# Kernel tuning notes

Measured on AMD Instinct MI355X. Metric: run time of the kernel, lower is better.

The kernel has to match this reference:

```python
import jax, jax.numpy as jnp
import numpy as np

L = 4        # routed layers
E = 12       # experts
NH = 4       # attention heads
C = 256      # hidden_dim
M = 128      # mlp_dim
TOPK = 1
LN_EPS = 1e-5


def setup_inputs() -> dict:
    key = jax.random.key(0)
    ks = jax.random.split(key, 16)
    B, H, W = 128, 14, 14

    def w(k, shape, s=0.02):
        return jax.random.normal(k, shape, dtype=jnp.float32) * s

    return {
        'stem_out': jax.random.normal(ks[0], (B, C, H, W), dtype=jnp.float32),
        'gate_w': w(ks[1], (L, C, E)), 'gate_b': jnp.zeros((L, E), jnp.float32),
        'ln1_g': jnp.ones((L, E, C), jnp.float32), 'ln1_b': jnp.zeros((L, E, C), jnp.float32),
        'wq': w(ks[2], (L, E, C, C)), 'bq': jnp.zeros((L, E, C), jnp.float32),
        'wk': w(ks[3], (L, E, C, C)), 'bk': jnp.zeros((L, E, C), jnp.float32),
        'wv': w(ks[4], (L, E, C, C)), 'bv': jnp.zeros((L, E, C), jnp.float32),
        'wo': w(ks[5], (L, E, C, C)), 'bo': jnp.zeros((L, E, C), jnp.float32),
        'ln2_g': jnp.ones((L, E, C), jnp.float32), 'ln2_b': jnp.zeros((L, E, C), jnp.float32),
        'w1': w(ks[6], (L, E, C, M)), 'b1': jnp.zeros((L, E, M), jnp.float32),
        'w2': w(ks[7], (L, E, M, C)), 'b2': jnp.zeros((L, E, C), jnp.float32),
    }


def _ln(x, g, b):
    mu = x.mean(axis=-1, keepdims=True)
    var = ((x - mu) ** 2).mean(axis=-1, keepdims=True)
    return (x - mu) * jax.lax.rsqrt(var + LN_EPS) * g + b


def _vit_block(x, p):
    # x: (B, H, W, C); p: per-expert params (no expert axis)
    B, H, W, Cc = x.shape
    d = Cc // NH
    h = _ln(x, p['g1'], p['bb1'])
    q = h @ p['wq'] + p['bq']
    k = h @ p['wk'] + p['bk']
    v = h @ p['wv'] + p['bv']

    def split(t):  # (B,H,W,C) -> (B, NH, H, W, d)
        return jnp.transpose(t.reshape(B, H, W, NH, d), (0, 3, 1, 2, 4))

    q, k, v = split(q), split(k), split(v)
    # attention is computed PER ROW h (over the W axis), matching the
    # original matmul(q, k.transpose(-2,-1)) on b n h w d tensors
    scale = jnp.asarray(d, x.dtype) ** 0.5
    scores = jnp.einsum('bnhqd,bnhkd->bnhqk', q, k) / scale
    attn = jax.nn.softmax(scores, axis=-1)
    o = jnp.einsum('bnhqk,bnhkd->bnhqd', attn, v)
    o = jnp.transpose(o, (0, 2, 3, 1, 4)).reshape(B, H, W, Cc)
    o = o @ p['wo'] + p['bo']
    x = x + o
    m = _ln(x, p['g2'], p['bb2'])
    m = jax.nn.gelu(m @ p['w1'] + p['b1'], approximate=False) @ p['w2'] + p['b2']
    return x + m


def reference(stem_out, gate_w, gate_b, ln1_g, ln1_b, wq, bq, wk, bk, wv, bv,
              wo, bo, ln2_g, ln2_b, w1, b1, w2, b2):
    x = jnp.transpose(stem_out, (0, 2, 3, 1))  # (B, H, W, C)
    B = x.shape[0]
    outputs_map, probs_list, idx_list = [], [], []
    for li in range(L):
        router_in = x.mean(axis=(1, 2))                 # (B, C)
        logits = router_in @ gate_w[li] + gate_b[li]    # (B, E)
        all_probs = jax.nn.softmax(logits, axis=-1)
        tk_p, tk_i = jax.lax.top_k(all_probs, TOPK)
        tk_p = tk_p / (tk_p.sum(axis=-1, keepdims=True) + 1e-8)
        # dense combine weights (B, E): scatter top-k weights per batch row
        w_be = jnp.zeros((B, E), x.dtype).at[jnp.arange(B)[:, None], tk_i].add(tk_p)
        p_li = {'g1': ln1_g[li], 'bb1': ln1_b[li],
                'wq': wq[li], 'bq': bq[li], 'wk': wk[li], 'bk': bk[li],
                'wv': wv[li], 'bv': bv[li], 'wo': wo[li], 'bo': bo[li],
                'g2': ln2_g[li], 'bb2': ln2_b[li],
                'w1': w1[li], 'b1': b1[li], 'w2': w2[li], 'b2': b2[li]}
        expert_outs = jax.vmap(lambda pp: _vit_block(x, pp))(p_li)  # (E,B,H,W,C)
        x = jnp.einsum('ebhwc,be->bhwc', expert_outs, w_be)
        outputs_map.append(jax.lax.stop_gradient(x))
        probs_list.append(all_probs)
        idx_list.append(tk_i)
    return (jnp.stack(outputs_map, axis=0),          # (4, B, H, W, C)
            jnp.concatenate(probs_list, axis=0),     # (4B, E)
            jnp.concatenate(idx_list, axis=0))       # (4B, top_k)
```

## Files before the change

### kernel.cpp

```cpp
#include <hip/hip_runtime.h>
#include <hip/hip_bf16.h>

#define LNUM 4
#define ENUM 12
#define CH 256
#define MLP 128
#define HW 196
#define BNUM 128
#define ROWLEN 14
#define MTOT (BNUM * HW)
#define MAXT128 208
#define MAXT64 416

#define PK_WQ 0
#define PK_WK 786432
#define PK_WV 1572864
#define PK_WO 2359296
#define PK_W1 3145728
#define PK_W2 3538944
#define PK_TOTAL 3932160

using bf16x8 = __attribute__((ext_vector_type(8))) short;
using f32x4 = __attribute__((ext_vector_type(4))) float;

__device__ inline unsigned short f2bf(float v) {
  __hip_bfloat16 b = __float2bfloat16(v);
  return *reinterpret_cast<unsigned short*>(&b);
}
__device__ inline float bf2f(unsigned short u) {
  union { unsigned int i; float f; } cv;
  cv.i = ((unsigned int)u) << 16;
  return cv.f;
}
__device__ inline void split_bf(float v, unsigned short& hi, unsigned short& lo) {
  hi = f2bf(v);
  lo = f2bf(v - bf2f(hi));
}
__device__ inline void gload16(const void* g, void* l) {
  __builtin_amdgcn_global_load_lds(
      (const __attribute__((address_space(1))) unsigned int*)g,
      (__attribute__((address_space(3))) unsigned int*)l, 16, 0, 0);
}

__global__ __launch_bounds__(256) void transpose_stem(const float* __restrict__ stem,
                                                      float* __restrict__ x,
                                                      int* __restrict__ rcnt) {
  if (blockIdx.x == 0 && blockIdx.y == 0 && blockIdx.z == 0 &&
      threadIdx.x == 0 && threadIdx.y == 0)
    rcnt[0] = 0;
  __shared__ float tile[32][33];
  int b = blockIdx.z;
  int c0 = blockIdx.x * 32;
  int p0 = blockIdx.y * 32;
  int tx = threadIdx.x;
  int ty = threadIdx.y;
  for (int i = ty; i < 32; i += 8) {
    int c = c0 + i, p = p0 + tx;
    if (p < HW) tile[i][tx] = stem[(size_t)b * CH * HW + (size_t)c * HW + p];
  }
  __syncthreads();
  for (int i = ty; i < 32; i += 8) {
    int p = p0 + i, c = c0 + tx;
    if (p < HW) x[(size_t)b * HW * CH + (size_t)p * CH + c] = tile[tx][i];
  }
}

__global__ __launch_bounds__(256) void router_kernel(
    const float* __restrict__ x, const float* __restrict__ gate_w,
    const float* __restrict__ gate_b, float* __restrict__ probs_out,
    float* __restrict__ idx_out, float* __restrict__ weight,
    int* __restrict__ eidx, int* __restrict__ rcnt, int* __restrict__ perm,
    int* __restrict__ te128, int* __restrict__ tr0128, int* __restrict__ trw128,
    int* __restrict__ te64, int* __restrict__ tr064, int* __restrict__ trw64,
    int li) {
  int b = blockIdx.x;
  int tid = threadIdx.x;
  int w = tid >> 6, lane = tid & 63;
  const float* xb = x + (size_t)b * HW * CH;
  float a0 = 0.f, a1 = 0.f, a2 = 0.f, a3 = 0.f;
#pragma unroll 7
  for (int i = 0; i < 49; ++i) {
    int p = w * 49 + i;
    float4 vv = *reinterpret_cast<const float4*>(&xb[(size_t)p * CH + lane * 4]);
    a0 += vv.x; a1 += vv.y; a2 += vv.z; a3 += vv.w;
  }
  __shared__ float rsum[4][CH];
  rsum[w][lane * 4 + 0] = a0;
  rsum[w][lane * 4 + 1] = a1;
  rsum[w][lane * 4 + 2] = a2;
  rsum[w][lane * 4 + 3] = a3;
  __syncthreads();
  __shared__ float r[CH];
  r[tid] = (rsum[0][tid] + rsum[1][tid] + rsum[2][tid] + rsum[3][tid]) *
           (1.0f / (float)HW);
  __syncthreads();
  __shared__ float part[ENUM][16];
  if (tid < 192) {
    int e = tid >> 4, seg = tid & 15;
    const float* gw = gate_w + (size_t)li * CH * ENUM;
    float acc = 0.f;
#pragma unroll
    for (int kk = 0; kk < 16; ++kk) {
      int k = seg * 16 + kk;
      acc += r[k] * gw[(size_t)k * ENUM + e];
    }
    part[e][seg] = acc;
  }
  __syncthreads();
  __shared__ float logits[ENUM];
  if (tid < ENUM) {
    float acc = gate_b[li * ENUM + tid];
#pragma unroll
    for (int seg = 0; seg < 16; ++seg) acc += part[tid][seg];
    logits[tid] = acc;
  }
  __syncthreads();
  __shared__ int last;
  if (tid == 0) {
    float mx = logits[0]; int am = 0;
    for (int e = 1; e < ENUM; ++e) if (logits[e] > mx) { mx = logits[e]; am = e; }
    float pr[ENUM]; float den = 0.f;
    for (int e = 0; e < ENUM; ++e) { pr[e] = expf(logits[e] - mx); den += pr[e]; }
    float inv = 1.0f / den;
    for (int e = 0; e < ENUM; ++e) pr[e] *= inv;
    for (int e = 0; e < ENUM; ++e)
      probs_out[(size_t)(li * BNUM + b) * ENUM + e] = pr[e];
    idx_out[li * BNUM + b] = (float)am;
    float pmax = pr[am];
    weight[b] = pmax / (pmax + 1e-8f);
    eidx[b] = am;
    __threadfence();
    int old = atomicAdd(rcnt, 1);
    last = (old == BNUM - 1) ? 1 : 0;
  }
  __syncthreads();
  if (!last) return;
  __threadfence();
  __shared__ int cnt[ENUM], start[ENUM];
  int t = tid;
  if (t < ENUM) {
    int cc = 0;
    for (int bb = 0; bb < BNUM; ++bb) if (eidx[bb] == t) ++cc;
    cnt[t] = cc;
  }
  __syncthreads();
  if (t == 0) {
    int ss = 0;
    for (int e = 0; e < ENUM; ++e) { start[e] = ss; ss += cnt[e]; }
  }
  __syncthreads();
  if (t < ENUM) {
    int pos = start[t];
    for (int bb = 0; bb < BNUM; ++bb) if (eidx[bb] == t) perm[pos++] = bb;
  }
  if (t == 0) {
    int tile = 0;
    for (int e = 0; e < ENUM; ++e) {
      int rows = cnt[e] * HW;
      int row0 = start[e] * HW;
      int off = 0;
      while (off < rows) {
        te128[tile] = e;
        tr0128[tile] = row0 + off;
        int rem = rows - off;
        trw128[tile] = rem < 128 ? rem : 128;
        ++tile; off += 128;
      }
    }
    for (; tile < MAXT128; ++tile) { trw128[tile] = 0; te128[tile] = 0; tr0128[tile] = 0; }
    rcnt[0] = 0;
  } else if (t == 1) {
    int tile = 0;
    for (int e = 0; e < ENUM; ++e) {
      int rows = cnt[e] * HW;
      int row0 = start[e] * HW;
      int off = 0;
      while (off < rows) {
        te64[tile] = e;
        tr064[tile] = row0 + off;
        int rem = rows - off;
        trw64[tile] = rem < 64 ? rem : 64;
        ++tile; off += 64;
      }
    }
    for (; tile < MAXT64; ++tile) { trw64[tile] = 0; te64[tile] = 0; tr064[tile] = 0; }
  }
}

__global__ __launch_bounds__(256) void prepack(
    const float* __restrict__ wq, const float* __restrict__ wk,
    const float* __restrict__ wv, const float* __restrict__ wo,
    const float* __restrict__ w1, const float* __restrict__ w2,
    unsigned short* __restrict__ Phi, unsigned short* __restrict__ Plo,
    int li0, int plane_mult) {
  int lz = blockIdx.z / ENUM;
  int e = blockIdx.z % ENUM;
  int li = li0 + lz;
  size_t plane = (size_t)lz * plane_mult;
  int ts = blockIdx.y;
  int K = (ts == 5) ? 128 : 256;
  int N = (ts == 4) ? 128 : 256;
  int total = (K / 8) * N;
  int id = blockIdx.x * 256 + threadIdx.x;
  if (id >= total) return;
  const float* src;
  size_t dst0;
  switch (ts) {
    case 0: src = wq; dst0 = PK_WQ; break;
    case 1: src = wk; dst0 = PK_WK; break;
    case 2: src = wv; dst0 = PK_WV; break;
    case 3: src = wo; dst0 = PK_WO; break;
    case 4: src = w1; dst0 = PK_W1; break;
    default: src = w2; dst0 = PK_W2; break;
  }
  src += ((size_t)li * ENUM + e) * K * N;
  size_t dst = plane + dst0 + (size_t)e * K * N;
  int n = id % N;
  int kg = id / N;
  const float* sp = src + (size_t)kg * 8 * N + n;
  unsigned short hs[8], ls[8];
#pragma unroll
  for (int j = 0; j < 8; ++j) split_bf(sp[(size_t)j * N], hs[j], ls[j]);
  uint4 ph, pl;
  ph.x = hs[0] | ((unsigned)hs[1] << 16); ph.y = hs[2] | ((unsigned)hs[3] << 16);
  ph.z = hs[4] | ((unsigned)hs[5] << 16); ph.w = hs[6] | ((unsigned)hs[7] << 16);
  pl.x = ls[0] | ((unsigned)ls[1] << 16); pl.y = ls[2] | ((unsigned)ls[3] << 16);
  pl.z = ls[4] | ((unsigned)ls[5] << 16); pl.w = ls[6] | ((unsigned)ls[7] << 16);
  size_t o = dst + (size_t)(kg * N + n) * 8;
  *reinterpret_cast<uint4*>(Phi + o) = ph;
  *reinterpret_cast<uint4*>(Plo + o) = pl;
}

__global__ __launch_bounds__(256) void ln_kernel(
    const float* __restrict__ xin, unsigned short* __restrict__ hhi,
    unsigned short* __restrict__ hlo,
    const float* __restrict__ g, const float* __restrict__ bta,
    const int* __restrict__ eidx, const int* __restrict__ perm, int li) {
  int tok = blockIdx.x * 4 + (threadIdx.x >> 6);
  int lane = threadIdx.x & 63;
  int s = tok / HW, p = tok - s * HW;
  int b = perm[s];
  int e = eidx[b];
  float4 vx = *reinterpret_cast<const float4*>(
      &xin[((size_t)b * HW + p) * CH + lane * 4]);
  float sm = vx.x + vx.y + vx.z + vx.w;
#pragma unroll
  for (int off = 1; off < 64; off <<= 1) sm += __shfl_xor(sm, off, 64);
  float mu = sm * (1.0f / (float)CH);
  float d0 = vx.x - mu, d1 = vx.y - mu, d2 = vx.z - mu, d3 = vx.w - mu;
  float s2 = d0 * d0 + d1 * d1 + d2 * d2 + d3 * d3;
#pragma unroll
  for (int off = 1; off < 64; off <<= 1) s2 += __shfl_xor(s2, off, 64);
  float rs = rsqrtf(s2 * (1.0f / (float)CH) + 1e-5f);
  size_t gb = ((size_t)li * ENUM + e) * CH + lane * 4;
  float4 gg = *reinterpret_cast<const float4*>(&g[gb]);
  float4 bb = *reinterpret_cast<const float4*>(&bta[gb]);
  float h0 = d0 * rs * gg.x + bb.x;
  float h1 = d1 * rs * gg.y + bb.y;
  float h2 = d2 * rs * gg.z + bb.z;
  float h3 = d3 * rs * gg.w + bb.w;
  ushort4 vh, vl;
  split_bf(h0, vh.x, vl.x);
  split_bf(h1, vh.y, vl.y);
  split_bf(h2, vh.z, vl.z);
  split_bf(h3, vh.w, vl.w);
  size_t ob = (size_t)tok * CH + lane * 4;
  *reinterpret_cast<ushort4*>(&hhi[ob]) = vh;
  *reinterpret_cast<ushort4*>(&hlo[ob]) = vl;
}

template <int EPI, int NT, int KDIM, int NXTOT, int TM_, int NTILE>
__global__ __launch_bounds__(256) void gemm_mfma(
    const unsigned short* __restrict__ Ahi, const unsigned short* __restrict__ Alo,
    const unsigned short* __restrict__ Whi, const unsigned short* __restrict__ Wlo,
    size_t wbase, size_t wstride,
    const float* __restrict__ B0, const float* __restrict__ B1p, const float* __restrict__ B2p,
    float* __restrict__ O0, float* __restrict__ O1p, float* __restrict__ O2p,
    unsigned short* __restrict__ Omhi, unsigned short* __restrict__ Omlo,
    float* __restrict__ X, const float* __restrict__ wgt,
    const int* __restrict__ tile_e, const int* __restrict__ tile_row0,
    const int* __restrict__ tile_rows, const int* __restrict__ perm, int li) {
  constexpr int NX = NT / 128;
  constexpr int NSTEP = KDIM / 32;
  constexpr int FM = TM_ / 32;
  constexpr int NSEG = TM_ / 64;
  int nwg = NXTOT * NTILE;
  int orig = blockIdx.x;
  int q = nwg >> 3, r = nwg & 7;
  int xcd = orig & 7, idx = orig >> 3;
  int wg = (xcd < r ? xcd * (q + 1) : r * (q + 1) + (xcd - r) * q) + idx;
  int tileid = wg / NXTOT;
  int cbx = wg % NXTOT;

  int rows = tile_rows[tileid];
  if (rows <= 0) return;
  int row0 = tile_row0[tileid];
  int e = tile_e[tileid];
  int cb = cbx / NX;
  int ncol0 = (cbx % NX) * 128;

  const float* Bt = (EPI == 0) ? (cb == 0 ? B0 : (cb == 1 ? B1p : B2p)) : B0;
  float* Oo = (EPI == 0) ? (cb == 0 ? O0 : (cb == 1 ? O1p : O2p)) : O0;
  size_t woff = wbase + (size_t)cb * wstride + (size_t)e * (KDIM * NT);
  const unsigned short* Wh = Whi + woff;
  const unsigned short* Wl = Wlo + woff;
  const float* bias = Bt + ((size_t)li * ENUM + e) * NT + ncol0;

  __shared__ unsigned short Ash[4][TM_][8], Asl[4][TM_][8];
  __shared__ unsigned short Bsh[4][128][8], Bsl[4][128][8];

  int tid = threadIdx.x;
  int lane = tid & 63, w = tid >> 6;
  int wr = w >> 1, wc = w & 1;
  int r0w = wr * (TM_ / 2), c0w = wc * 64;
  int lrow = lane & 15, lk = lane >> 4;

  const unsigned short* gAh[NSEG];
  const unsigned short* gAl[NSEG];
#pragma unroll
  for (int s = 0; s < NSEG; ++s) {
    int rl = (s * 64 + lane < rows) ? s * 64 + lane : 0;
    gAh[s] = Ahi + (size_t)(row0 + rl) * KDIM + w * 8;
    gAl[s] = Alo + (size_t)(row0 + rl) * KDIM + w * 8;
  }

  f32x4 acc[FM][4];
#pragma unroll
  for (int i = 0; i < FM; ++i)
#pragma unroll
    for (int j = 0; j < 4; ++j) acc[i][j] = (f32x4){0.f, 0.f, 0.f, 0.f};

#pragma unroll
  for (int t = 0; t < NSTEP; ++t) {
    int k0 = t * 32;
#pragma unroll
    for (int s = 0; s < NSEG; ++s) {
      gload16(gAh[s] + k0, &Ash[w][s * 64][0]);
      gload16(gAl[s] + k0, &Asl[w][s * 64][0]);
    }
    const unsigned short* gBh = Wh + ((size_t)(t * 4 + w) * NT + ncol0 + lane) * 8;
    const unsigned short* gBl = Wl + ((size_t)(t * 4 + w) * NT + ncol0 + lane) * 8;
    gload16(gBh, &Bsh[w][0][0]);
    gload16(gBh + 64 * 8, &Bsh[w][64][0]);
    gload16(gBl, &Bsl[w][0][0]);
    gload16(gBl + 64 * 8, &Bsl[w][64][0]);
    __syncthreads();
    bf16x8 bh[4], bl[4];
#pragma unroll
    for (int fj = 0; fj < 4; ++fj) {
      bh[fj] = *reinterpret_cast<const bf16x8*>(&Bsh[lk][c0w + fj * 16 + lrow][0]);
      bl[fj] = *reinterpret_cast<const bf16x8*>(&Bsl[lk][c0w + fj * 16 + lrow][0]);
    }
#pragma unroll
    for (int fi = 0; fi < FM; ++fi) {
      bf16x8 ah = *reinterpret_cast<const bf16x8*>(&Ash[lk][r0w + fi * 16 + lrow][0]);
      bf16x8 al = *reinterpret_cast<const bf16x8*>(&Asl[lk][r0w + fi * 16 + lrow][0]);
#pragma unroll
      for (int fj = 0; fj < 4; ++fj) {
        acc[fi][fj] = __builtin_amdgcn_mfma_f32_16x16x32_bf16(ah, bh[fj], acc[fi][fj], 0, 0, 0);
        acc[fi][fj] = __builtin_amdgcn_mfma_f32_16x16x32_bf16(ah, bl[fj], acc[fi][fj], 0, 0, 0);
        acc[fi][fj] = __builtin_amdgcn_mfma_f32_16x16x32_bf16(al, bh[fj], acc[fi][fj], 0, 0, 0);
      }
    }
    __syncthreads();
  }

#pragma unroll
  for (int fi = 0; fi < FM; ++fi) {
#pragma unroll
    for (int r2 = 0; r2 < 4; ++r2) {
      int row_l = r0w + fi * 16 + lk * 4 + r2;
      if (row_l >= rows) continue;
      int rg = row0 + row_l;
      int bsrt = 0; size_t gxb = 0; float wr_ = 1.f;
      if (EPI >= 2) {
        int s = rg / HW, p = rg - s * HW;
        bsrt = perm[s];
        gxb = ((size_t)bsrt * HW + p) * CH;
        if (EPI == 3) wr_ = wgt[bsrt];
      }
#pragma unroll
      for (int fj = 0; fj < 4; ++fj) {
        int col = c0w + fj * 16 + lrow;
        int ocol = ncol0 + col;
        float v = acc[fi][fj][r2] + bias[col];
        if (EPI == 0) {
          Oo[(size_t)rg * NT + ocol] = v;
        } else if (EPI == 1) {
          float gl = 0.5f * v * (1.0f + erff(v * 0.70710678118654752f));
          unsigned short hi, lo;
          split_bf(gl, hi, lo);
          Omhi[(size_t)rg * MLP + ocol] = hi;
          Omlo[(size_t)rg * MLP + ocol] = lo;
        } else if (EPI == 2) {
          X[gxb + ocol] += v;
        } else {
          float vv = (v + X[gxb + ocol]) * wr_;
          X[gxb + ocol] = vv;
          O0[gxb + ocol] = vv;
        }
      }
    }
  }
}

__global__ __launch_bounds__(256) void attn_kernel(
    const float* __restrict__ q, const float* __restrict__ k,
    const float* __restrict__ v, unsigned short* __restrict__ ohi,
    unsigned short* __restrict__ olo) {
  int br = blockIdx.x;
  int b = br / ROWLEN, row = br % ROWLEN;
  size_t base = ((size_t)b * HW + (size_t)row * ROWLEN) * CH;
  __shared__ float qs[ROWLEN][CH + 4];
  __shared__ float ks[ROWLEN][CH + 4];
  __shared__ float vs[ROWLEN][CH + 4];
  __shared__ float sc[4][ROWLEN][ROWLEN];
  int tid = threadIdx.x;
  for (int idx = tid; idx < ROWLEN * 64; idx += 256) {
    int rr = idx >> 6, c4 = (idx & 63) * 4;
    size_t go = base + (size_t)rr * CH + c4;
    float4 qv = *reinterpret_cast<const float4*>(&q[go]);
    float4 kv = *reinterpret_cast<const float4*>(&k[go]);
    float4 vv = *reinterpret_cast<const float4*>(&v[go]);
    *reinterpret_cast<float4*>(&qs[rr][c4]) = qv;
    *reinterpret_cast<float4*>(&ks[rr][c4]) = kv;
    *reinterpret_cast<float4*>(&vs[rr][c4]) = vv;
  }
  __syncthreads();
  for (int sidx = tid; sidx < 4 * ROWLEN * ROWLEN; sidx += 256) {
    int n = sidx / (ROWLEN * ROWLEN);
    int rem = sidx % (ROWLEN * ROWLEN);
    int i = rem / ROWLEN, j = rem % ROWLEN;
    const float* qp = &qs[i][n * 64];
    const float* kp = &ks[j][n * 64];
    float s = 0.f;
#pragma unroll
    for (int d = 0; d < 64; ++d) s = fmaf(qp[d], kp[d], s);
    sc[n][i][j] = s * 0.125f;
  }
  __syncthreads();
  if (tid < 4 * ROWLEN) {
    int n = tid / ROWLEN, i = tid % ROWLEN;
    float mx = sc[n][i][0];
    for (int j = 1; j < ROWLEN; ++j) mx = fmaxf(mx, sc[n][i][j]);
    float ex[ROWLEN]; float den = 0.f;
    for (int j = 0; j < ROWLEN; ++j) { ex[j] = expf(sc[n][i][j] - mx); den += ex[j]; }
    float inv = 1.0f / den;
    for (int j = 0; j < ROWLEN; ++j) sc[n][i][j] = ex[j] * inv;
  }
  __syncthreads();
  int n = tid / 64;
  for (int i = 0; i < ROWLEN; ++i) {
    float s = 0.f;
#pragma unroll
    for (int j = 0; j < ROWLEN; ++j) s = fmaf(sc[n][i][j], vs[j][tid], s);
    unsigned short hi, lo;
    split_bf(s, hi, lo);
    ohi[base + (size_t)i * CH + tid] = hi;
    olo[base + (size_t)i * CH + tid] = lo;
  }
}

extern "C" void kernel_launch(void* const* d_in, const int* in_sizes, int n_in,
                              void* d_out, int out_size, void* d_ws, size_t ws_size,
                              hipStream_t stream) {
  const float* stem = (const float*)d_in[0];
  const float* gate_w = (const float*)d_in[1];
  const float* gate_b = (const float*)d_in[2];
  const float* ln1_g = (const float*)d_in[3];
  const float* ln1_b = (const float*)d_in[4];
  const float* wq = (const float*)d_in[5];
  const float* bq = (const float*)d_in[6];
  const float* wk = (const float*)d_in[7];
  const float* bk = (const float*)d_in[8];
  const float* wv = (const float*)d_in[9];
  const float* bv = (const float*)d_in[10];
  const float* wo = (const float*)d_in[11];
  const float* bo = (const float*)d_in[12];
  const float* ln2_g = (const float*)d_in[13];
  const float* ln2_b = (const float*)d_in[14];
  const float* w1 = (const float*)d_in[15];
  const float* b1 = (const float*)d_in[16];
  const float* w2 = (const float*)d_in[17];
  const float* b2 = (const float*)d_in[18];

  float* out = (float*)d_out;
  float* ws = (float*)d_ws;
  const size_t IMG = (size_t)BNUM * HW * CH;
  float* x = ws;
  unsigned short* h_hi = (unsigned short*)(ws + IMG);
  unsigned short* h_lo = h_hi + (size_t)MTOT * CH;
  float* q = ws + 2 * IMG;
  float* k = ws + 3 * IMG;
  float* v = ws + 4 * IMG;
  unsigned short* m_hi = (unsigned short*)q;
  unsigned short* m_lo = m_hi + (size_t)MTOT * MLP;
  float* weight = ws + 5 * IMG;
  int* ip = (int*)(weight + BNUM);
  int* eidx = ip;              ip += BNUM;
  int* perm = ip;              ip += BNUM;
  int* te128 = ip;             ip += MAXT128;
  int* tr0128 = ip;            ip += MAXT128;
  int* trw128 = ip;            ip += MAXT128;
  int* te64 = ip;              ip += MAXT64;
  int* tr064 = ip;             ip += MAXT64;
  int* trw64 = ip;             ip += MAXT64;
  int* rcnt = ip;              ip += 4;
  unsigned short* Whi_p = (unsigned short*)(ws + 5 * IMG + 4096);

  const size_t base_bytes = (5 * IMG + 4096) * sizeof(float);
  const int all_mode = (ws_size >= base_bytes + (size_t)4 * PK_TOTAL * 2 * sizeof(unsigned short)) ? 1 : 0;
  const int nplane = all_mode ? LNUM : 1;
  unsigned short* Wlo_p = Whi_p + (size_t)nplane * PK_TOTAL;

  float* probs_out = out + 4 * IMG;
  float* idx_out = probs_out + (size_t)LNUM * BNUM * ENUM;

  transpose_stem<<<dim3(8, 7, BNUM), dim3(32, 8), 0, stream>>>(stem, x, rcnt);
  if (all_mode) {
    prepack<<<dim3(32, 6, ENUM * LNUM), 256, 0, stream>>>(
        wq, wk, wv, wo, w1, w2, Whi_p, Wlo_p, 0, PK_TOTAL);
  }

  for (int li = 0; li < LNUM; ++li) {
    router_kernel<<<BNUM, 256, 0, stream>>>(
        x, gate_w, gate_b, probs_out, idx_out, weight, eidx, rcnt, perm,
        te128, tr0128, trw128, te64, tr064, trw64, li);
    if (!all_mode) {
      prepack<<<dim3(32, 6, ENUM), 256, 0, stream>>>(
          wq, wk, wv, wo, w1, w2, Whi_p, Wlo_p, li, 0);
    }
    size_t plane = all_mode ? (size_t)li * PK_TOTAL : 0;
    ln_kernel<<<MTOT / 4, 256, 0, stream>>>(x, h_hi, h_lo, ln1_g, ln1_b, eidx, perm, li);
    gemm_mfma<0, 256, 256, 6, 128, MAXT128><<<dim3(6 * MAXT128), 256, 0, stream>>>(
        h_hi, h_lo, Whi_p, Wlo_p, plane + PK_WQ, (size_t)(ENUM * CH * CH),
        bq, bk, bv, q, k, v, nullptr, nullptr, nullptr, nullptr,
        te128, tr0128, trw128, perm, li);
    attn_kernel<<<BNUM * ROWLEN, 256, 0, stream>>>(q, k, v, h_hi, h_lo);
    gemm_mfma<2, 256, 256, 2, 64, MAXT64><<<dim3(2 * MAXT64), 256, 0, stream>>>(
        h_hi, h_lo, Whi_p, Wlo_p, plane + PK_WO, 0,
        bo, nullptr, nullptr, nullptr, nullptr, nullptr, nullptr, nullptr,
        x, nullptr, te64, tr064, trw64, perm, li);
    ln_kernel<<<MTOT / 4, 256, 0, stream>>>(x, h_hi, h_lo, ln2_g, ln2_b, eidx, perm, li);
    gemm_mfma<1, 128, 256, 1, 64, MAXT64><<<dim3(1 * MAXT64), 256, 0, stream>>>(
        h_hi, h_lo, Whi_p, Wlo_p, plane + PK_W1, 0,
        b1, nullptr, nullptr, nullptr, nullptr, nullptr, m_hi, m_lo,
        nullptr, nullptr, te64, tr064, trw64, perm, li);
    gemm_mfma<3, 256, 128, 2, 64, MAXT64><<<dim3(2 * MAXT64), 256, 0, stream>>>(
        m_hi, m_lo, Whi_p, Wlo_p, plane + PK_W2, 0,
        b2, nullptr, nullptr, out + (size_t)li * IMG, nullptr, nullptr,
        nullptr, nullptr, x, weight, te64, tr064, trw64, perm, li);
  }
}
```

Measured before the change: 880.9 us.

## Fuse MLP up-projection, GELU and down-projection into one kernel

Replaces the two MLP GEMM launches with a single fused kernel per 64-row tile. The GELU output is kept in shared memory as split-bf16 hi/lo instead of round-tripping through global memory. The down-projection then runs over the full 256 output columns in that block, and the generic GEMM template drops its MLP epilogues. This removes one launch and the intermediate global traffic, at the cost of 64KB of shared memory per block and fewer workgroups (one per tile instead of two for W2), which may lower occupancy and parallelism.

```diff
diff --git a/kernel.cpp b/kernel.cpp
--- a/kernel.cpp
+++ b/kernel.cpp
@@ -276,8 +276,7 @@
     size_t wbase, size_t wstride,
     const float* __restrict__ B0, const float* __restrict__ B1p, const float* __restrict__ B2p,
     float* __restrict__ O0, float* __restrict__ O1p, float* __restrict__ O2p,
-    unsigned short* __restrict__ Omhi, unsigned short* __restrict__ Omlo,
-    float* __restrict__ X, const float* __restrict__ wgt,
+    float* __restrict__ X,
     const int* __restrict__ tile_e, const int* __restrict__ tile_row0,
     const int* __restrict__ tile_rows, const int* __restrict__ perm, int li) {
   constexpr int NX = NT / 128;
@@ -372,12 +371,10 @@
       int row_l = r0w + fi * 16 + lk * 4 + r2;
       if (row_l >= rows) continue;
       int rg = row0 + row_l;
-      int bsrt = 0; size_t gxb = 0; float wr_ = 1.f;
-      if (EPI >= 2) {
+      size_t gxb = 0;
+      if (EPI == 2) {
         int s = rg / HW, p = rg - s * HW;
-        bsrt = perm[s];
-        gxb = ((size_t)bsrt * HW + p) * CH;
-        if (EPI == 3) wr_ = wgt[bsrt];
+        gxb = ((size_t)perm[s] * HW + p) * CH;
       }
 #pragma unroll
       for (int fj = 0; fj < 4; ++fj) {
@@ -386,19 +383,172 @@
         float v = acc[fi][fj][r2] + bias[col];
         if (EPI == 0) {
           Oo[(size_t)rg * NT + ocol] = v;
-        } else if (EPI == 1) {
-          float gl = 0.5f * v * (1.0f + erff(v * 0.70710678118654752f));
-          unsigned short hi, lo;
-          split_bf(gl, hi, lo);
-          Omhi[(size_t)rg * MLP + ocol] = hi;
-          Omlo[(size_t)rg * MLP + ocol] = lo;
-        } else if (EPI == 2) {
+        } else {
           X[gxb + ocol] += v;
-        } else {
-          float vv = (v + X[gxb + ocol]) * wr_;
-          X[gxb + ocol] = vv;
-          O0[gxb + ocol] = vv;
         }
+      }
+    }
+  }
+}
+
+__global__ __launch_bounds__(256) void fused_mlp(
+    const unsigned short* __restrict__ Ahi, const unsigned short* __restrict__ Alo,
+    const unsigned short* __restrict__ Whi, const unsigned short* __restrict__ Wlo,
+    size_t plane, const float* __restrict__ b1, const float* __restrict__ b2,
+    float* __restrict__ Oout, float* __restrict__ X, const float* __restrict__ wgt,
+    const int* __restrict__ tile_e, const int* __restrict__ tile_row0,
+    const int* __restrict__ tile_rows, const int* __restrict__ perm, int li) {
+  int nwg = MAXT64;
+  int orig = blockIdx.x;
+  int q = nwg >> 3, r = nwg & 7;
+  int xcd = orig & 7, idx = orig >> 3;
+  int tileid = (xcd < r ? xcd * (q + 1) : r * (q + 1) + (xcd - r) * q) + idx;
+
+  int rows = tile_rows[tileid];
+  if (rows <= 0) return;
+  int row0 = tile_row0[tileid];
+  int e = tile_e[tileid];
+
+  const unsigned short* W1h = Whi + plane + PK_W1 + (size_t)e * (CH * MLP);
+  const unsigned short* W1l = Wlo + plane + PK_W1 + (size_t)e * (CH * MLP);
+  const unsigned short* W2h = Whi + plane + PK_W2 + (size_t)e * (MLP * CH);
+  const unsigned short* W2l = Wlo + plane + PK_W2 + (size_t)e * (MLP * CH);
+  const float* bias1 = b1 + ((size_t)li * ENUM + e) * MLP;
+  const float* bias2 = b2 + ((size_t)li * ENUM + e) * CH;
+
+  __shared__ __align__(16) unsigned short smem[32768];
+  unsigned short* Am_h = smem;
+  unsigned short* Am_l = smem + 8192;
+  unsigned short* S = smem + 16384;
+  unsigned short* Ash = S;
+  unsigned short* Asl = S + 2048;
+  unsigned short* Bsh = S + 4096;
+  unsigned short* Bsl = S + 8192;
+  unsigned short* B2h = S;
+  unsigned short* B2l = S + 8192;
+
+  int tid = threadIdx.x;
+  int lane = tid & 63, w = tid >> 6;
+  int wr = w >> 1, wc = w & 1;
+  int r0w = wr * 32, c0w = wc * 64;
+  int lrow = lane & 15, lk = lane >> 4;
+
+  int rl = (lane < rows) ? lane : 0;
+  const unsigned short* gAh = Ahi + (size_t)(row0 + rl) * CH + w * 8;
+  const unsigned short* gAl = Alo + (size_t)(row0 + rl) * CH + w * 8;
+
+  f32x4 acc1[2][4];
+#pragma unroll
+  for (int i = 0; i < 2; ++i)
+#pragma unroll
+    for (int j = 0; j < 4; ++j) acc1[i][j] = (f32x4){0.f, 0.f, 0.f, 0.f};
+
+#pragma unroll
+  for (int t = 0; t < 8; ++t) {
+    int k0 = t * 32;
+    gload16(gAh + k0, Ash + w * 512);
+    gload16(gAl + k0, Asl + w * 512);
+    const unsigned short* gBh = W1h + ((size_t)(t * 4 + w) * MLP + lane) * 8;
+    const unsigned short* gBl = W1l + ((size_t)(t * 4 + w) * MLP + lane) * 8;
+    gload16(gBh, Bsh + w * 1024);
+    gload16(gBh + 64 * 8, Bsh + w * 1024 + 64 * 8);
+    gload16(gBl, Bsl + w * 1024);
+    gload16(gBl + 64 * 8, Bsl + w * 1024 + 64 * 8);
+    __syncthreads();
+    bf16x8 bh[4], bl[4];
+#pragma unroll
+    for (int fj = 0; fj < 4; ++fj) {
+      bh[fj] = *reinterpret_cast<const bf16x8*>(Bsh + lk * 1024 + (c0w + fj * 16 + lrow) * 8);
+      bl[fj] = *reinterpret_cast<const bf16x8*>(Bsl + lk * 1024 + (c0w + fj * 16 + lrow) * 8);
+    }
+#pragma unroll
+    for (int fi = 0; fi < 2; ++fi) {
+      bf16x8 ah = *reinterpret_cast<const bf16x8*>(Ash + lk * 512 + (r0w + fi * 16 + lrow) * 8);
+      bf16x8 al = *reinterpret_cast<const bf16x8*>(Asl + lk * 512 + (r0w + fi * 16 + lrow) * 8);
+#pragma unroll
+      for (int fj = 0; fj < 4; ++fj) {
+        acc1[fi][fj] = __builtin_amdgcn_mfma_f32_16x16x32_bf16(ah, bh[fj], acc1[fi][fj], 0, 0, 0);
+        acc1[fi][fj] = __builtin_amdgcn_mfma_f32_16x16x32_bf16(ah, bl[fj], acc1[fi][fj], 0, 0, 0);
+        acc1[fi][fj] = __builtin_amdgcn_mfma_f32_16x16x32_bf16(al, bh[fj], acc1[fi][fj], 0, 0, 0);
+      }
+    }
+    __syncthreads();
+  }
+
+#pragma unroll
+  for (int fi = 0; fi < 2; ++fi) {
+#pragma unroll
+    for (int r2 = 0; r2 < 4; ++r2) {
+      int row = r0w + fi * 16 + lk * 4 + r2;
+#pragma unroll
+      for (int fj = 0; fj < 4; ++fj) {
+        int col = c0w + fj * 16 + lrow;
+        float v = acc1[fi][fj][r2] + bias1[col];
+        float gl = 0.5f * v * (1.0f + erff(v * 0.70710678118654752f));
+        unsigned short hi, lo;
+        split_bf(gl, hi, lo);
+        int o = (col >> 3) * 512 + row * 8 + (col & 7);
+        Am_h[o] = hi;
+        Am_l[o] = lo;
+      }
+    }
+  }
+  __syncthreads();
+
+  f32x4 acc2[2][8];
+#pragma unroll
+  for (int i = 0; i < 2; ++i)
+#pragma unroll
+    for (int j = 0; j < 8; ++j) acc2[i][j] = (f32x4){0.f, 0.f, 0.f, 0.f};
+  int c0w2 = wc * 128;
+
+#pragma unroll
+  for (int t = 0; t < 4; ++t) {
+    const unsigned short* gBh = W2h + ((size_t)(t * 4 + w) * CH + lane) * 8;
+    const unsigned short* gBl = W2l + ((size_t)(t * 4 + w) * CH + lane) * 8;
+#pragma unroll
+    for (int s = 0; s < 4; ++s) {
+      gload16(gBh + s * 64 * 8, B2h + w * 2048 + s * 64 * 8);
+      gload16(gBl + s * 64 * 8, B2l + w * 2048 + s * 64 * 8);
+    }
+    __syncthreads();
+    bf16x8 bh[8], bl[8];
+#pragma unroll
+    for (int fj = 0; fj < 8; ++fj) {
+      bh[fj] = *reinterpret_cast<const bf16x8*>(B2h + lk * 2048 + (c0w2 + fj * 16 + lrow) * 8);
+      bl[fj] = *reinterpret_cast<const bf16x8*>(B2l + lk * 2048 + (c0w2 + fj * 16 + lrow) * 8);
+    }
+#pragma unroll
+    for (int fi = 0; fi < 2; ++fi) {
+      bf16x8 ah = *reinterpret_cast<const bf16x8*>(Am_h + (t * 4 + lk) * 512 + (r0w + fi * 16 + lrow) * 8);
+      bf16x8 al = *reinterpret_cast<const bf16x8*>(Am_l + (t * 4 + lk) * 512 + (r0w + fi * 16 + lrow) * 8);
+#pragma unroll
+      for (int fj = 0; fj < 8; ++fj) {
+        acc2[fi][fj] = __builtin_amdgcn_mfma_f32_16x16x32_bf16(ah, bh[fj], acc2[fi][fj], 0, 0, 0);
+        acc2[fi][fj] = __builtin_amdgcn_mfma_f32_16x16x32_bf16(ah, bl[fj], acc2[fi][fj], 0, 0, 0);
+        acc2[fi][fj] = __builtin_amdgcn_mfma_f32_16x16x32_bf16(al, bh[fj], acc2[fi][fj], 0, 0, 0);
+      }
+    }
+    __syncthreads();
+  }
+
+#pragma unroll
+  for (int fi = 0; fi < 2; ++fi) {
+#pragma unroll
+    for (int r2 = 0; r2 < 4; ++r2) {
+      int row_l = r0w + fi * 16 + lk * 4 + r2;
+      if (row_l >= rows) continue;
+      int rg = row0 + row_l;
+      int s = rg / HW, p = rg - s * HW;
+      int bsrt = perm[s];
+      size_t gxb = ((size_t)bsrt * HW + p) * CH;
+      float wr_ = wgt[bsrt];
+#pragma unroll
+      for (int fj = 0; fj < 8; ++fj) {
+        int ocol = c0w2 + fj * 16 + lrow;
+        float vv = (acc2[fi][fj][r2] + bias2[ocol] + X[gxb + ocol]) * wr_;
+        X[gxb + ocol] = vv;
+        Oout[gxb + ocol] = vv;
       }
     }
   }
@@ -493,8 +643,6 @@
   float* q = ws + 2 * IMG;
   float* k = ws + 3 * IMG;
   float* v = ws + 4 * IMG;
-  unsigned short* m_hi = (unsigned short*)q;
-  unsigned short* m_lo = m_hi + (size_t)MTOT * MLP;
   float* weight = ws + 5 * IMG;
   int* ip = (int*)(weight + BNUM);
   int* eidx = ip;              ip += BNUM;
@@ -534,21 +682,16 @@
     ln_kernel<<<MTOT / 4, 256, 0, stream>>>(x, h_hi, h_lo, ln1_g, ln1_b, eidx, perm, li);
     gemm_mfma<0, 256, 256, 6, 128, MAXT128><<<dim3(6 * MAXT128), 256, 0, stream>>>(
         h_hi, h_lo, Whi_p, Wlo_p, plane + PK_WQ, (size_t)(ENUM * CH * CH),
-        bq, bk, bv, q, k, v, nullptr, nullptr, nullptr, nullptr,
+        bq, bk, bv, q, k, v, nullptr,
         te128, tr0128, trw128, perm, li);
     attn_kernel<<<BNUM * ROWLEN, 256, 0, stream>>>(q, k, v, h_hi, h_lo);
     gemm_mfma<2, 256, 256, 2, 64, MAXT64><<<dim3(2 * MAXT64), 256, 0, stream>>>(
         h_hi, h_lo, Whi_p, Wlo_p, plane + PK_WO, 0,
-        bo, nullptr, nullptr, nullptr, nullptr, nullptr, nullptr, nullptr,
-        x, nullptr, te64, tr064, trw64, perm, li);
+        bo, nullptr, nullptr, nullptr, nullptr, nullptr,
+        x, te64, tr064, trw64, perm, li);
     ln_kernel<<<MTOT / 4, 256, 0, stream>>>(x, h_hi, h_lo, ln2_g, ln2_b, eidx, perm, li);
-    gemm_mfma<1, 128, 256, 1, 64, MAXT64><<<dim3(1 * MAXT64), 256, 0, stream>>>(
-        h_hi, h_lo, Whi_p, Wlo_p, plane + PK_W1, 0,
-        b1, nullptr, nullptr, nullptr, nullptr, nullptr, m_hi, m_lo,
-        nullptr, nullptr, te64, tr064, trw64, perm, li);
-    gemm_mfma<3, 256, 128, 2, 64, MAXT64><<<dim3(2 * MAXT64), 256, 0, stream>>>(
-        m_hi, m_lo, Whi_p, Wlo_p, plane + PK_W2, 0,
-        b2, nullptr, nullptr, out + (size_t)li * IMG, nullptr, nullptr,
-        nullptr, nullptr, x, weight, te64, tr064, trw64, perm, li);
-  }
-}
+    fused_mlp<<<dim3(MAXT64), 256, 0, stream>>>(
+        h_hi, h_lo, Whi_p, Wlo_p, plane, b1, b2, out + (size_t)li * IMG,
+        x, weight, te64, tr064, trw64, perm, li);
+  }
+}
```

After: 844.3 us (median of 2 runs). 4.2% less time.
